# Kernel tuning notes

Hardware: AMD Instinct MI355X
Metric: run time of the kernel (lower is better)

The kernel has to match this reference:

```python
import jax, jax.numpy as jnp
import numpy as np

SEQ_LEN = 252; WIN = 96; LEADS = 12; SECONDS = 10
LAYERS = 12; HEADS = 8; E = 128; FF = 512; B = 128
S = SEQ_LEN + LEADS  # 264 tokens after cls_token concat


def setup_inputs() -> dict:
    key = jax.random.key(0)
    ks = jax.random.split(key, 16)
    def n(k, shape, s=0.02):
        return jax.random.normal(k, shape, jnp.float32) * s
    return {
        "x": jax.random.normal(ks[0], (B, SEQ_LEN, WIN), jnp.float32),
        "t_indices": jax.random.randint(ks[1], (B, SEQ_LEN), 0, SECONDS + 1),
        "spatial_indices": jax.random.randint(ks[2], (B, SEQ_LEN), 0, LEADS + 1),
        "conv_w": n(ks[3], (E, WIN)),          # Conv1d k=1 == linear over window dim
        "conv_b": n(ks[4], (E,)),
        "pos_embed": n(ks[5], (1, S, E)),
        "time_tab": n(ks[6], (SECONDS + 1, E)),  # stacked time_embed_set
        "spat_tab": n(ks[7], (LEADS + 1, E)),    # stacked sqatial_embed_set
        "cls_token": n(ks[8], (1, LEADS, E)),
        "Wqkv": n(ks[9], (LAYERS, 3 * E, E)), "bqkv": jnp.zeros((LAYERS, 3 * E)),
        "Wo": n(ks[10], (LAYERS, E, E)), "bo": jnp.zeros((LAYERS, E)),
        "W1": n(ks[11], (LAYERS, FF, E)), "b1": jnp.zeros((LAYERS, FF)),
        "W2": n(ks[12], (LAYERS, E, FF)), "b2": jnp.zeros((LAYERS, E)),
        "ln1_g": jnp.ones((LAYERS, E)), "ln1_b": jnp.zeros((LAYERS, E)),
        "ln2_g": jnp.ones((LAYERS, E)), "ln2_b": jnp.zeros((LAYERS, E)),
    }


def _ln(x, g, b, eps=1e-5):
    m = x.mean(-1, keepdims=True)
    v = ((x - m) ** 2).mean(-1, keepdims=True)
    return (x - m) * jax.lax.rsqrt(v + eps) * g + b


def reference(x, t_indices, spatial_indices, conv_w, conv_b, pos_embed,
              time_tab, spat_tab, cls_token, Wqkv, bqkv, Wo, bo,
              W1, b1, W2, b2, ln1_g, ln1_b, ln2_g, ln2_b):
    Bn = x.shape[0]
    D = E // HEADS
    # kernel-size-1 Conv1d over window channels == per-token linear
    h = jnp.einsum('blt,et->ble', x, conv_w) + conv_b        # [B, L, E]
    h = jnp.concatenate([jnp.broadcast_to(cls_token, (Bn, LEADS, E)), h], axis=1)
    h = h + pos_embed                                        # [B, S, E]
    # vectorized replacement of the B*L python-loop gather
    h = h.at[:, LEADS:, :].add(time_tab[t_indices] + spat_tab[spatial_indices])
    # dropout: eval mode (identity)
    for i in range(LAYERS):  # post-norm TransformerEncoderLayer, relu FFN
        qkv = h @ Wqkv[i].T + bqkv[i]
        q, k, v = jnp.split(qkv, 3, axis=-1)
        q = q.reshape(Bn, S, HEADS, D)
        k = k.reshape(Bn, S, HEADS, D)
        v = v.reshape(Bn, S, HEADS, D)
        att = jax.nn.softmax(jnp.einsum('bqhd,bkhd->bhqk', q, k) / np.sqrt(D).astype(np.float32), axis=-1)
        o = jnp.einsum('bhqk,bkhd->bqhd', att, v).reshape(Bn, S, E) @ Wo[i].T + bo[i]
        h = _ln(h + o, ln1_g[i], ln1_b[i])
        ff = jax.nn.relu(h @ W1[i].T + b1[i]) @ W2[i].T + b2[i]
        h = _ln(h + ff, ln2_g[i], ln2_b[i])
    return h
```

## Files before the change

### kernel.cpp

```cpp
#include <hip/hip_runtime.h>

typedef unsigned short u16;
typedef __attribute__((ext_vector_type(8))) short s16x8;
typedef __attribute__((ext_vector_type(4))) float f32x4;

__device__ __forceinline__ float bf2f(u16 u) {
    union { unsigned i; float f; } v; v.i = (unsigned)u << 16; return v.f;
}
__device__ __forceinline__ u16 f2bf(float f) {
    union { float f; unsigned i; } v; v.f = f;
    unsigned r = v.i + 0x7fffu + ((v.i >> 16) & 1u);
    return (u16)(r >> 16);
}
__device__ __forceinline__ unsigned fbits(float f) {
    union { float f; unsigned i; } v; v.f = f; return v.i;
}
__device__ __forceinline__ f32x4 mfma16(s16x8 a, s16x8 b, f32x4 c) {
    return __builtin_amdgcn_mfma_f32_16x16x32_bf16(a, b, c, 0, 0, 0);
}

__global__ __launch_bounds__(256)
void cvt_kernel(const float* __restrict__ src, u16* __restrict__ dst, int n)
{
    for (int i = blockIdx.x * 256 + threadIdx.x; i < n; i += gridDim.x * 256)
        dst[i] = f2bf(src[i]);
}

__global__ __launch_bounds__(256)
void embed_cls_kernel(const float* __restrict__ cls, const float* __restrict__ pos,
                      u16* __restrict__ h16)
{
    int i = blockIdx.x * 256 + threadIdx.x;
    int e = i & 127, s = (i >> 7) % 12, b = i / (12 * 128);
    float v = cls[s * 128 + e] + pos[s * 128 + e];
    h16[((size_t)b * 264 + s) * 128 + e] = f2bf(v);
}

__global__ __launch_bounds__(256)
void embed_mfma(const u16* __restrict__ x16, const u16* __restrict__ cw16,
                const float* __restrict__ cb, const float* __restrict__ pos,
                const float* __restrict__ ttab, const float* __restrict__ stab,
                const int* __restrict__ tidx, const int* __restrict__ sidx,
                u16* __restrict__ h16)
{
    const int t = threadIdx.x;
    const int wave = t >> 6, lane = t & 63;
    const int quad = lane >> 4, l16 = lane & 15;
    const int n0 = wave * 32;

    s16x8 wf[2][3];
    float bv[2];
    #pragma unroll
    for (int nt = 0; nt < 2; ++nt) {
        bv[nt] = cb[n0 + nt * 16 + l16];
        #pragma unroll
        for (int ks = 0; ks < 3; ++ks)
            wf[nt][ks] = *(const s16x8*)&cw16[(n0 + nt * 16 + l16) * 96 + ks * 32 + quad * 8];
    }
    #pragma unroll
    for (int tt = 0; tt < 4; ++tt) {
        const int m0 = (blockIdx.x * 4 + tt) * 16;
        s16x8 af[3];
        #pragma unroll
        for (int ks = 0; ks < 3; ++ks)
            af[ks] = *(const s16x8*)&x16[(size_t)(m0 + l16) * 96 + ks * 32 + quad * 8];
        f32x4 a0 = (f32x4){0.f,0.f,0.f,0.f}, a1 = (f32x4){0.f,0.f,0.f,0.f};
        #pragma unroll
        for (int ks = 0; ks < 3; ++ks) {
            a0 = mfma16(af[ks], wf[0][ks], a0);
            a1 = mfma16(af[ks], wf[1][ks], a1);
        }
        #pragma unroll
        for (int r = 0; r < 4; ++r) {
            int row = m0 + quad * 4 + r;
            int b = row / 252, l = row - b * 252;
            int ti = tidx[row], si = sidx[row];
            size_t tok = (size_t)b * 264 + 12 + l;
            #pragma unroll
            for (int nt = 0; nt < 2; ++nt) {
                int col = n0 + nt * 16 + l16;
                float v = (nt ? a1[r] : a0[r]) + bv[nt]
                        + pos[(12 + l) * 128 + col]
                        + ttab[ti * 128 + col] + stab[si * 128 + col];
                h16[tok * 128 + col] = f2bf(v);
            }
        }
    }
}

template<bool RELU, bool QSCALE>
__global__ __launch_bounds__(256)
void gemm_bias(const u16* __restrict__ A, const u16* __restrict__ W,
               const float* __restrict__ bias, u16* __restrict__ C,
               int N, int K)
{
    const int LDK = 136;
    __shared__ alignas(16) u16 As[64 * 136];
    __shared__ alignas(16) u16 Ws[64 * 136];
    const int m0 = blockIdx.x * 64;
    const int n0 = blockIdx.y * 64;
    const int t = threadIdx.x;
    const int wave = t >> 6, lane = t & 63;
    const int quad = lane >> 4, l16 = lane & 15;
    const int wm = (wave & 1) * 32, wn = (wave >> 1) * 32;

    f32x4 acc[2][2];
    #pragma unroll
    for (int i = 0; i < 2; ++i)
        #pragma unroll
        for (int j = 0; j < 2; ++j) acc[i][j] = (f32x4){0.f, 0.f, 0.f, 0.f};

    for (int kc = 0; kc < K; kc += 128) {
        __syncthreads();
        #pragma unroll
        for (int i = 0; i < 4; ++i) {
            int id = i * 256 + t;
            int row = id >> 4, c8 = (id & 15) << 3;
            *(uint4*)&As[row * LDK + c8] = *(const uint4*)&A[(size_t)(m0 + row) * K + kc + c8];
            *(uint4*)&Ws[row * LDK + c8] = *(const uint4*)&W[(size_t)(n0 + row) * K + kc + c8];
        }
        __syncthreads();
        #pragma unroll
        for (int ks = 0; ks < 4; ++ks) {
            s16x8 a0 = *(const s16x8*)&As[(wm + l16) * LDK + ks * 32 + quad * 8];
            s16x8 a1 = *(const s16x8*)&As[(wm + 16 + l16) * LDK + ks * 32 + quad * 8];
            s16x8 b0 = *(const s16x8*)&Ws[(wn + l16) * LDK + ks * 32 + quad * 8];
            s16x8 b1 = *(const s16x8*)&Ws[(wn + 16 + l16) * LDK + ks * 32 + quad * 8];
            acc[0][0] = mfma16(a0, b0, acc[0][0]);
            acc[0][1] = mfma16(a0, b1, acc[0][1]);
            acc[1][0] = mfma16(a1, b0, acc[1][0]);
            acc[1][1] = mfma16(a1, b1, acc[1][1]);
        }
    }
    #pragma unroll
    for (int ni = 0; ni < 2; ++ni) {
        int col = n0 + wn + ni * 16 + l16;
        float bv = bias[col];
        #pragma unroll
        for (int mi = 0; mi < 2; ++mi) {
            #pragma unroll
            for (int r = 0; r < 4; ++r) {
                int row = m0 + wm + mi * 16 + quad * 4 + r;
                float v = acc[mi][ni][r] + bv;
                if (RELU) v = fmaxf(v, 0.f);
                if (QSCALE && blockIdx.y < 2) v *= 0.360673760222241f;
                C[(size_t)row * N + col] = f2bf(v);
            }
        }
    }
}

template<int K, bool W32>
__global__ __launch_bounds__(256)
void gemm_ln(const u16* __restrict__ A, const u16* __restrict__ W,
             const float* __restrict__ bias, const u16* __restrict__ resid,
             const float* __restrict__ g, const float* __restrict__ be,
             float* o32, u16* o16)
{
    const int LDK = 136;
    __shared__ alignas(16) u16 As[64 * 136];
    __shared__ alignas(16) u16 Ws[128 * 136];
    const int m0 = blockIdx.x * 64;
    const int t = threadIdx.x;
    const int wave = t >> 6, lane = t & 63;
    const int quad = lane >> 4, l16 = lane & 15;
    const int wr = wave * 16;

    f32x4 acc[8];
    #pragma unroll
    for (int i = 0; i < 8; ++i) acc[i] = (f32x4){0.f, 0.f, 0.f, 0.f};

    for (int kc = 0; kc < K; kc += 128) {
        __syncthreads();
        #pragma unroll
        for (int i = 0; i < 4; ++i) {
            int id = i * 256 + t;
            int row = id >> 4, c8 = (id & 15) << 3;
            *(uint4*)&As[row * LDK + c8] = *(const uint4*)&A[(size_t)(m0 + row) * K + kc + c8];
        }
        #pragma unroll
        for (int i = 0; i < 8; ++i) {
            int id = i * 256 + t;
            int row = id >> 4, c8 = (id & 15) << 3;
            *(uint4*)&Ws[row * LDK + c8] = *(const uint4*)&W[(size_t)row * K + kc + c8];
        }
        __syncthreads();
        #pragma unroll
        for (int ks = 0; ks < 4; ++ks) {
            s16x8 a = *(const s16x8*)&As[(wr + l16) * LDK + ks * 32 + quad * 8];
            #pragma unroll
            for (int nt = 0; nt < 8; ++nt) {
                s16x8 b = *(const s16x8*)&Ws[(nt * 16 + l16) * LDK + ks * 32 + quad * 8];
                acc[nt] = mfma16(a, b, acc[nt]);
            }
        }
    }
    #pragma unroll
    for (int nt = 0; nt < 8; ++nt) {
        int col = nt * 16 + l16;
        float bv = bias[col];
        #pragma unroll
        for (int r = 0; r < 4; ++r) {
            int row = m0 + wr + quad * 4 + r;
            acc[nt][r] += bv + bf2f(resid[(size_t)row * 128 + col]);
        }
    }
    float sm[4], sq[4];
    #pragma unroll
    for (int r = 0; r < 4; ++r) {
        float s = 0.f, q = 0.f;
        #pragma unroll
        for (int nt = 0; nt < 8; ++nt) { float v = acc[nt][r]; s += v; q += v * v; }
        sm[r] = s; sq[r] = q;
    }
    #pragma unroll
    for (int mk = 1; mk < 16; mk <<= 1) {
        #pragma unroll
        for (int r = 0; r < 4; ++r) {
            sm[r] += __shfl_xor(sm[r], mk, 64);
            sq[r] += __shfl_xor(sq[r], mk, 64);
        }
    }
    #pragma unroll
    for (int r = 0; r < 4; ++r) {
        float mean = sm[r] * (1.f / 128.f);
        float var = sq[r] * (1.f / 128.f) - mean * mean;
        float rstd = rsqrtf(var + 1e-5f);
        int row = m0 + wr + quad * 4 + r;
        #pragma unroll
        for (int nt = 0; nt < 8; ++nt) {
            int col = nt * 16 + l16;
            float y = (acc[nt][r] - mean) * rstd * g[col] + be[col];
            if (W32) o32[(size_t)row * 128 + col] = y;
            else     o16[(size_t)row * 128 + col] = f2bf(y);
        }
    }
}

__global__ __launch_bounds__(256)
void attn_kernel(const u16* __restrict__ qkv, u16* __restrict__ ctx)
{
    const int STR = 296;
    const int KLD = 24;
    __shared__ alignas(16) u16 VT[16 * STR];
    __shared__ alignas(16) u16 Ks[272 * KLD];
    const int b = blockIdx.x >> 3, h = blockIdx.x & 7;
    const size_t base = (size_t)b * 264 * 384;
    const int t = threadIdx.x;
    const int wave = t >> 6, lane = t & 63;
    const int quad = lane >> 4, l16 = lane & 15;
    const int hq = h * 16;

    for (int i = t; i < 264 * 2; i += 256) {
        int key = i >> 1, dq = (i & 1) * 8;
        *(uint4*)&Ks[key * KLD + dq] =
            *(const uint4*)&qkv[base + (size_t)key * 384 + 128 + hq + dq];
    }
    for (int i = t; i < 264 * 16; i += 256) {
        int s = i >> 4, d = i & 15;
        VT[d * STR + s] = qkv[base + (size_t)s * 384 + 256 + hq + d];
    }
    for (int i = t; i < 16 * 32; i += 256) {
        int d = i >> 5, c = 264 + (i & 31);
        VT[d * STR + c] = 0;
    }
    __syncthreads();

    for (int qt = wave; qt < 17; qt += 4) {
        const int q0 = qt * 16;
        s16x8 qf = (s16x8){0, 0, 0, 0, 0, 0, 0, 0};
        {
            int qrow = q0 + l16;
            if (quad < 2 && qrow < 264)
                qf = *(const s16x8*)&qkv[base + (size_t)qrow * 384 + hq + quad * 8];
        }
        f32x4 sc[17];
        #pragma unroll
        for (int kt = 0; kt < 17; ++kt) {
            s16x8 kf = (s16x8){0, 0, 0, 0, 0, 0, 0, 0};
            if (quad < 2)
                kf = *(const s16x8*)&Ks[(kt * 16 + l16) * KLD + quad * 8];
            f32x4 z = (f32x4){0.f, 0.f, 0.f, 0.f};
            sc[kt] = mfma16(kf, qf, z);
        }
        float mx = -1e30f;
        #pragma unroll
        for (int kt = 0; kt < 17; ++kt) {
            #pragma unroll
            for (int r = 0; r < 4; ++r) {
                float s = sc[kt][r];
                if (kt == 16 && quad >= 2) s = -1e30f;
                sc[kt][r] = s;
                mx = fmaxf(mx, s);
            }
        }
        mx = fmaxf(mx, __shfl_xor(mx, 16, 64));
        mx = fmaxf(mx, __shfl_xor(mx, 32, 64));
        float ls = 0.f;
        #pragma unroll
        for (int kt = 0; kt < 17; ++kt) {
            #pragma unroll
            for (int r = 0; r < 4; ++r) {
                float e = __builtin_amdgcn_exp2f(sc[kt][r] - mx);
                sc[kt][r] = e;
                ls += e;
            }
        }
        ls += __shfl_xor(ls, 16, 64);
        ls += __shfl_xor(ls, 32, 64);
        float rinv = 1.f / ls;
        float rinvT[4];
        #pragma unroll
        for (int r = 0; r < 4; ++r) rinvT[r] = __shfl(rinv, quad * 4 + r, 64);

        f32x4 oa = (f32x4){0.f, 0.f, 0.f, 0.f};
        #pragma unroll
        for (int c = 0; c < 9; ++c) {
            const int kt0 = 2 * c, kt1 = 2 * c + 1;
            union { s16x8 v; uint4 w; } pk;
            pk.w.x = __builtin_amdgcn_perm(fbits(sc[kt0][1]), fbits(sc[kt0][0]), 0x07060302u);
            pk.w.y = __builtin_amdgcn_perm(fbits(sc[kt0][3]), fbits(sc[kt0][2]), 0x07060302u);
            if (c == 8) { pk.w.z = 0; pk.w.w = 0; }
            else {
                pk.w.z = __builtin_amdgcn_perm(fbits(sc[kt1][1]), fbits(sc[kt1][0]), 0x07060302u);
                pk.w.w = __builtin_amdgcn_perm(fbits(sc[kt1][3]), fbits(sc[kt1][2]), 0x07060302u);
            }
            union { s16x8 v; uint2 h2[2]; } vt;
            vt.h2[0] = *(const uint2*)&VT[l16 * STR + kt0 * 16 + quad * 4];
            vt.h2[1] = *(const uint2*)&VT[l16 * STR + kt1 * 16 + quad * 4];
            oa = mfma16(pk.v, vt.v, oa);
        }
        #pragma unroll
        for (int r = 0; r < 4; ++r) {
            int row = q0 + quad * 4 + r;
            if (row < 264)
                ctx[((size_t)b * 264 + row) * 128 + hq + l16] = f2bf(oa[r] * rinvT[r]);
        }
    }
}

extern "C" void kernel_launch(void* const* d_in, const int* in_sizes, int n_in,
                              void* d_out, int out_size, void* d_ws, size_t ws_size,
                              hipStream_t stream)
{
    (void)in_sizes; (void)n_in; (void)out_size; (void)ws_size;
    const float* x    = (const float*)d_in[0];
    const int*   tidx = (const int*)d_in[1];
    const int*   sidx = (const int*)d_in[2];
    const float* cw   = (const float*)d_in[3];
    const float* cb   = (const float*)d_in[4];
    const float* pos  = (const float*)d_in[5];
    const float* ttab = (const float*)d_in[6];
    const float* stab = (const float*)d_in[7];
    const float* cls  = (const float*)d_in[8];
    const float* Wqkv = (const float*)d_in[9];
    const float* bqkv = (const float*)d_in[10];
    const float* Wo   = (const float*)d_in[11];
    const float* bo   = (const float*)d_in[12];
    const float* W1   = (const float*)d_in[13];
    const float* b1   = (const float*)d_in[14];
    const float* W2   = (const float*)d_in[15];
    const float* b2   = (const float*)d_in[16];
    const float* g1   = (const float*)d_in[17];
    const float* be1  = (const float*)d_in[18];
    const float* g2   = (const float*)d_in[19];
    const float* be2  = (const float*)d_in[20];

    char* ws = (char*)d_ws;
    u16* h16    = (u16*)ws;
    u16* hA     = (u16*)(ws + 8650752);
    u16* big    = (u16*)(ws + 17301504);
    u16* ctx    = (u16*)(ws + 51904512);
    u16* wqkv16 = (u16*)(ws + 60555264);
    u16* wo16   = (u16*)(ws + 61734912);
    u16* w116   = (u16*)(ws + 62128128);
    u16* w216   = (u16*)(ws + 63700992);
    u16* x16    = big;
    u16* cw16   = ctx;

    cvt_kernel<<<512, 256, 0, stream>>>(Wqkv, wqkv16, 12 * 384 * 128);
    cvt_kernel<<<256, 256, 0, stream>>>(Wo,   wo16,   12 * 128 * 128);
    cvt_kernel<<<512, 256, 0, stream>>>(W1,   w116,   12 * 512 * 128);
    cvt_kernel<<<512, 256, 0, stream>>>(W2,   w216,   12 * 128 * 512);
    cvt_kernel<<<1024, 256, 0, stream>>>(x,   x16,    128 * 252 * 96);
    cvt_kernel<<<48, 256, 0, stream>>>(cw,    cw16,   128 * 96);
    embed_cls_kernel<<<768, 256, 0, stream>>>(cls, pos, h16);
    embed_mfma<<<504, 256, 0, stream>>>(x16, cw16, cb, pos, ttab, stab, tidx, sidx, h16);

    for (int l = 0; l < 12; ++l) {
        gemm_bias<false, true><<<dim3(528, 6), 256, 0, stream>>>(
            h16, wqkv16 + l * 384 * 128, bqkv + l * 384, big, 384, 128);
        attn_kernel<<<1024, 256, 0, stream>>>(big, ctx);
        gemm_ln<128, false><<<528, 256, 0, stream>>>(
            ctx, wo16 + l * 128 * 128, bo + l * 128, h16, g1 + l * 128, be1 + l * 128,
            nullptr, hA);
        gemm_bias<true, false><<<dim3(528, 8), 256, 0, stream>>>(
            hA, w116 + l * 512 * 128, b1 + l * 512, big, 512, 128);
        if (l == 11) {
            gemm_ln<512, true><<<528, 256, 0, stream>>>(
                big, w216 + l * 128 * 512, b2 + l * 128, hA, g2 + l * 128, be2 + l * 128,
                (float*)d_out, nullptr);
        } else {
            gemm_ln<512, false><<<528, 256, 0, stream>>>(
                big, w216 + l * 128 * 512, b2 + l * 128, hA, g2 + l * 128, be2 + l * 128,
                nullptr, h16);
        }
    }
}
```

Measured before the change: 1.192 ms.

## Store QKV in head-major planes so attention loads contiguous per-head tiles

```diff
diff --git a/kernel.cpp b/kernel.cpp
--- a/kernel.cpp
+++ b/kernel.cpp
@@ -18,6 +18,8 @@
 __device__ __forceinline__ f32x4 mfma16(s16x8 a, s16x8 b, f32x4 c) {
     return __builtin_amdgcn_mfma_f32_16x16x32_bf16(a, b, c, 0, 0, 0);
 }
+
+#define PLANE 4325376
 
 __global__ __launch_bounds__(256)
 void cvt_kernel(const float* __restrict__ src, u16* __restrict__ dst, int n)
@@ -88,7 +90,7 @@
     }
 }
 
-template<bool RELU, bool QSCALE>
+template<bool RELU, bool QSCALE, bool QKVL>
 __global__ __launch_bounds__(256)
 void gemm_bias(const u16* __restrict__ A, const u16* __restrict__ W,
                const float* __restrict__ bias, u16* __restrict__ C,
@@ -144,7 +146,13 @@
                 float v = acc[mi][ni][r] + bv;
                 if (RELU) v = fmaxf(v, 0.f);
                 if (QSCALE && blockIdx.y < 2) v *= 0.360673760222241f;
-                C[(size_t)row * N + col] = f2bf(v);
+                if (QKVL) {
+                    int part = col >> 7, hh = (col >> 4) & 7, d = col & 15;
+                    int b = row / 264, s = row - b * 264;
+                    C[(size_t)part * PLANE + (size_t)b * 33792 + hh * 4224 + s * 16 + d] = f2bf(v);
+                } else {
+                    C[(size_t)row * N + col] = f2bf(v);
+                }
             }
         }
     }
@@ -245,20 +253,25 @@
     __shared__ alignas(16) u16 VT[16 * STR];
     __shared__ alignas(16) u16 Ks[272 * KLD];
     const int b = blockIdx.x >> 3, h = blockIdx.x & 7;
-    const size_t base = (size_t)b * 264 * 384;
+    const u16* qp = qkv + (size_t)(b * 8 + h) * 4224;
+    const u16* kp = qp + PLANE;
+    const u16* vp = qp + 2 * PLANE;
     const int t = threadIdx.x;
     const int wave = t >> 6, lane = t & 63;
     const int quad = lane >> 4, l16 = lane & 15;
     const int hq = h * 16;
 
-    for (int i = t; i < 264 * 2; i += 256) {
+    for (int i = t; i < 528; i += 256)
+        *(uint4*)&Ks[(i >> 1) * KLD + (i & 1) * 8] = *(const uint4*)&kp[i * 8];
+    for (int i = t; i < 528; i += 256) {
         int key = i >> 1, dq = (i & 1) * 8;
-        *(uint4*)&Ks[key * KLD + dq] =
-            *(const uint4*)&qkv[base + (size_t)key * 384 + 128 + hq + dq];
-    }
-    for (int i = t; i < 264 * 16; i += 256) {
-        int s = i >> 4, d = i & 15;
-        VT[d * STR + s] = qkv[base + (size_t)s * 384 + 256 + hq + d];
+        union { uint4 w; u16 u[8]; } vv;
+        vv.w = *(const uint4*)&vp[i * 8];
+        #pragma unroll
+        for (int j = 0; j < 8; ++j) {
+            int jj = (i & 1) ? ((j + 4) & 7) : j;
+            VT[(dq + jj) * STR + key] = vv.u[jj];
+        }
     }
     for (int i = t; i < 16 * 32; i += 256) {
         int d = i >> 5, c = 264 + (i & 31);
@@ -272,7 +285,7 @@
         {
             int qrow = q0 + l16;
             if (quad < 2 && qrow < 264)
-                qf = *(const s16x8*)&qkv[base + (size_t)qrow * 384 + hq + quad * 8];
+                qf = *(const s16x8*)&qp[qrow * 16 + quad * 8];
         }
         f32x4 sc[17];
         #pragma unroll
@@ -388,13 +401,13 @@
     embed_mfma<<<504, 256, 0, stream>>>(x16, cw16, cb, pos, ttab, stab, tidx, sidx, h16);
 
     for (int l = 0; l < 12; ++l) {
-        gemm_bias<false, true><<<dim3(528, 6), 256, 0, stream>>>(
+        gemm_bias<false, true, true><<<dim3(528, 6), 256, 0, stream>>>(
             h16, wqkv16 + l * 384 * 128, bqkv + l * 384, big, 384, 128);
         attn_kernel<<<1024, 256, 0, stream>>>(big, ctx);
         gemm_ln<128, false><<<528, 256, 0, stream>>>(
             ctx, wo16 + l * 128 * 128, bo + l * 128, h16, g1 + l * 128, be1 + l * 128,
             nullptr, hA);
-        gemm_bias<true, false><<<dim3(528, 8), 256, 0, stream>>>(
+        gemm_bias<true, false, false><<<dim3(528, 8), 256, 0, stream>>>(
             hA, w116 + l * 512 * 128, b1 + l * 512, big, 512, 128);
         if (l == 11) {
             gemm_ln<512, true><<<528, 256, 0, stream>>>(
```

Measured after the change: 1.175 ms. No clear change (-1.4%).
